# Kernel optimization log

Hardware: AMD Instinct MI355X
Metric: run time of the kernel (lower is better)

Reference implementation:

```python
import jax, jax.numpy as jnp
import numpy as np

# norse LIFParameters defaults with method='super', alpha=100
TAU_SYN_INV = 200.0
TAU_MEM_INV = 100.0
V_LEAK = 0.0
V_TH = 1.0
V_RESET = 0.0
ALPHA = 100.0
DT = 0.001
SEQ_LENGTH = 100

@jax.custom_vjp
def super_spike(x):
    return (x > 0).astype(x.dtype)

def _ss_fwd(x):
    return super_spike(x), x

def _ss_bwd(x, g):
    # SuperSpike surrogate: dz/dx = 1 / (alpha*|x| + 1)^2
    return (g / (ALPHA * jnp.abs(x) + 1.0) ** 2,)

super_spike.defvjp(_ss_fwd, _ss_bwd)

def lif_step(inp, v, i):
    v_dec = v + DT * TAU_MEM_INV * ((V_LEAK - v) + i)
    i_dec = i * (1.0 - DT * TAU_SYN_INV)
    z = super_spike(v_dec - V_TH)
    v_new = (1.0 - z) * v_dec + z * V_RESET
    i_new = i_dec + inp
    return z, v_new, i_new

def setup_inputs() -> dict:
    key = jax.random.key(0)
    ks = jax.random.split(key, 5)
    B, F, H, C = 16384, 256, 256, 10
    x = jax.random.normal(ks[0], (B, F), dtype=jnp.float32)
    W_hidden = jax.random.normal(ks[1], (H, F), dtype=jnp.float32) / np.sqrt(F)
    b_hidden = jax.random.normal(ks[2], (H,), dtype=jnp.float32) * 0.01
    W_readout = jax.random.normal(ks[3], (C, H), dtype=jnp.float32) / np.sqrt(H)
    b_readout = jax.random.normal(ks[4], (C,), dtype=jnp.float32) * 0.01
    return {"x": x, "W_hidden": W_hidden, "b_hidden": b_hidden,
            "W_readout": W_readout, "b_readout": b_readout}

def reference(x, W_hidden, b_hidden, W_readout, b_readout):
    B, F = x.shape
    H = W_hidden.shape[0]
    z0 = jnp.zeros((B, F), x.dtype)
    z1 = jnp.zeros((B, H), x.dtype)

    def step(carry, _):
        v1, i1, v2, i2, acc = carry
        # input LIF cell (same input current x at every timestep)
        z, v1, i1 = lif_step(x, v1, i1)
        h = jnp.einsum('bf,hf->bh', z, W_hidden) + b_hidden
        # output LIF cell
        z2, v2, i2 = lif_step(h, v2, i2)
        return (v1, i1, v2, i2, acc + z2), None

    carry0 = (z0, z0, z1, z1, z1)
    (v1, i1, v2, i2, acc), _ = jax.lax.scan(step, carry0, None, length=SEQ_LENGTH)
    mean_spikes = acc / SEQ_LENGTH  # == outputs.mean(0)
    return jnp.einsum('bh,ch->bc', mean_spikes, W_readout) + b_readout
```

## Files before the change

### kernel.cpp

```cpp
#include <hip/hip_runtime.h>
#include <hip/hip_fp16.h>
#include <stdint.h>


#define BB 16384
#define FF 256
#define HH 256
#define CC 10
#define TT 100

typedef __attribute__((ext_vector_type(4))) int int4v;

__global__ __launch_bounds__(256) void spike_gen(
    const float* __restrict__ x, unsigned long long* __restrict__ Z) {
  const int lane = threadIdx.x & 63;
  const int wv   = threadIdx.x >> 6;
  const int b0   = blockIdx.x * 8 + wv * 2;
  const float K_VM = (float)(0.001 * 100.0);
  const float K_ID = (float)(1.0 - 0.001 * 200.0);

  float v[8], cur[8], xv[8];
#pragma unroll
  for (int jb = 0; jb < 2; ++jb)
#pragma unroll
    for (int js = 0; js < 4; ++js) {
      const int idx = jb * 4 + js;
      xv[idx] = x[(size_t)(b0 + jb) * FF + js * 64 + lane];
      v[idx] = 0.0f; cur[idx] = 0.0f;
    }

  const bool s0 = (lane & 1) != 0, s1 = (lane & 2) != 0, s2 = (lane & 4) != 0;
  unsigned long long* zp = Z + (size_t)b0 * 4;

  for (int t = 0; t < TT; ++t) {
    unsigned long long bal[8];
#pragma unroll
    for (int idx = 0; idx < 8; ++idx) {
      float vd   = __fadd_rn(v[idx], __fmul_rn(K_VM, __fadd_rn(-v[idx], cur[idx])));
      float idec = __fmul_rn(cur[idx], K_ID);
      bool z = (vd > 1.0f);
      bal[idx] = __ballot(z);
      v[idx]   = z ? 0.0f : vd;
      cur[idx] = __fadd_rn(idec, xv[idx]);
    }
    unsigned long long m0 = s0 ? bal[1] : bal[0];
    unsigned long long m1 = s0 ? bal[3] : bal[2];
    unsigned long long m2 = s0 ? bal[5] : bal[4];
    unsigned long long m3 = s0 ? bal[7] : bal[6];
    unsigned long long n0 = s1 ? m1 : m0;
    unsigned long long n1 = s1 ? m3 : m2;
    unsigned long long m  = s2 ? n1 : n0;
    if (lane < 8) zp[(size_t)t * (BB * 4) + lane] = m;
  }
}

__global__ __launch_bounds__(256, 4) void snn_main(
    const uint32_t* __restrict__ Z, const float* __restrict__ Wh,
    const float* __restrict__ bh, const float* __restrict__ Wr,
    const float* __restrict__ br, float* __restrict__ out) {
  __shared__ __align__(16) char WS[32768];

  const int tid = threadIdx.x;
  const int bx  = blockIdx.x;
  const int hc  = bx & 3;
  const int bc  = bx >> 2;
  const int h0  = hc * 64;
  const int b0  = bc * 64;

  {
    int4v* ws4 = (int4v*)WS;
#pragma unroll
    for (int half = 0; half < 4; ++half) {
      const int u  = tid + half * 256;
      const int rr = u >> 4;
      const int q  = u & 15;
      const int s  = q >> 2, kq = q & 3;
      const int nt = rr >> 4, n = rr & 15;
      const float* wp = Wh + (size_t)(h0 + rr) * FF + s * 64 + kq * 16;
      uint32_t pa[4], pb[4];
#pragma unroll
      for (int c4 = 0; c4 < 4; ++c4) {
        float4 w4 = *(const float4*)(wp + c4 * 4);
        float wf[4] = {w4.x, w4.y, w4.z, w4.w};
        uint32_t ua = 0, ub = 0;
#pragma unroll
        for (int e = 0; e < 4; ++e) {
          float af = rintf(wf[e] * 256.0f);
          af = fminf(fmaxf(af, -127.0f), 127.0f);
          float bf = rintf(__builtin_fmaf(af, -64.0f, wf[e] * 16384.0f));
          bf = fminf(fmaxf(bf, -127.0f), 127.0f);
          ua |= ((uint32_t)((int)af) & 255u) << (8 * e);
          ub |= ((uint32_t)((int)bf) & 255u) << (8 * e);
        }
        pa[c4] = ua; pb[c4] = ub;
      }
      ws4[((nt * 2 + 0) * 4 + s) * 64 + kq * 16 + n] = *(int4v*)pa;
      ws4[((nt * 2 + 1) * 4 + s) * 64 + kq * 16 + n] = *(int4v*)pb;
    }
  }
  __syncthreads();

  const int lane = tid & 63;
  const int bsub = tid >> 6;
  const int col  = lane & 15;
  const int quad = lane >> 4;
  const bool qhi = (quad & 2) != 0;
  const uint32_t shl16 = (quad & 1) * 16;

  const int brow = b0 + bsub * 16 + col;

  const float K_VM = (float)(0.001 * 100.0);
  const float K_ID = (float)(1.0 - 0.001 * 200.0);

  float v2[4][4], ii[4][4];
  uint32_t sc[4];
#pragma unroll
  for (int nt = 0; nt < 4; ++nt) {
    sc[nt] = 0u;
#pragma unroll
    for (int r = 0; r < 4; ++r) { v2[nt][r] = 0.f; ii[nt][r] = 0.f; }
  }

  float bias[4];
#pragma unroll
  for (int nt = 0; nt < 4; ++nt) bias[nt] = bh[h0 + nt * 16 + col];

  uint32_t hwS0[2], hwS1[2], hwS2[2], hwS3[2];
  const uint32_t* zrow = Z + (size_t)brow * 8;

  auto load_hw = [&](int tgi) {
#pragma unroll
    for (int j = 0; j < 2; ++j) {
      const uint32_t* p = zrow + ((size_t)tgi * 2 + j) * (size_t)(BB * 8);
      uint4 a = *(const uint4*)p;
      uint4 b4 = *(const uint4*)(p + 4);
      hwS0[j] = (qhi ? a.y : a.x) >> shl16;
      hwS1[j] = (qhi ? a.w : a.z) >> shl16;
      hwS2[j] = (qhi ? b4.y : b4.x) >> shl16;
      hwS3[j] = (qhi ? b4.w : b4.z) >> shl16;
    }
  };
  load_hw(0);

  const char* wsl = WS + lane * 16;

#pragma unroll 1
  for (int tg = 0; tg < TT / 2; ++tg) {
    int4v acc[2][4];
#pragma unroll
    for (int j = 0; j < 2; ++j)
#pragma unroll
      for (int nt = 0; nt < 4; ++nt)
        acc[j][nt] = (int4v){0, 0, 0, 0};

#pragma unroll 1
    for (int s = 0; s < 4; ++s) {
      const int4v* bp = (const int4v*)(wsl + s * 1024);
      int4v Ba[4], Bb[4];
#pragma unroll
      for (int nt = 0; nt < 4; ++nt) {
        Ba[nt] = bp[(nt * 2 + 0) * 256];
        Bb[nt] = bp[(nt * 2 + 1) * 256];
      }
#pragma unroll
      for (int j = 0; j < 2; ++j) {
        uint32_t t0 = (s & 1) ? hwS1[j] : hwS0[j];
        uint32_t t1 = (s & 1) ? hwS3[j] : hwS2[j];
        uint32_t h16 = (s & 2) ? t1 : t0;
        int4v za, zb_;
#pragma unroll
        for (int p = 0; p < 4; ++p) {
          uint32_t nib = (h16 >> (4 * p)) & 15u;
          uint32_t zbyte = __umul24(nib, 0x204081u) & 0x01010101u;
          zb_[p] = (int)zbyte;
          za[p]  = (int)(zbyte << 6);
        }
#pragma unroll
        for (int nt = 0; nt < 4; ++nt) {
          acc[j][nt] = __builtin_amdgcn_mfma_i32_16x16x64_i8(
              za, Ba[nt], acc[j][nt], 0, 0, 0);
          acc[j][nt] = __builtin_amdgcn_mfma_i32_16x16x64_i8(
              zb_, Bb[nt], acc[j][nt], 0, 0, 0);
        }
      }
    }

    if (tg < TT / 2 - 1) load_hw(tg + 1);

#pragma unroll
    for (int j = 0; j < 2; ++j) {
#pragma unroll
      for (int nt = 0; nt < 4; ++nt) {
#pragma unroll
        for (int r = 0; r < 4; ++r) {
          float h  = __builtin_fmaf((float)acc[j][nt][r], 6.103515625e-05f,
                                    bias[nt]);
          float vv = v2[nt][r], ci = ii[nt][r];
          float vd   = __fadd_rn(vv, __fmul_rn(K_VM, __fadd_rn(-vv, ci)));
          float idec = __fmul_rn(ci, K_ID);
          bool z = (vd > 1.0f);
          v2[nt][r] = z ? 0.0f : vd;
          ii[nt][r] = __fadd_rn(idec, h);
          sc[nt] += (z ? 1u : 0u) << (8 * r);
        }
      }
    }
  }

  float mean[4][4];
#pragma unroll
  for (int nt = 0; nt < 4; ++nt)
#pragma unroll
    for (int r = 0; r < 4; ++r)
      mean[nt][r] = __fdiv_rn((float)((sc[nt] >> (8 * r)) & 255u), 100.0f);

#pragma unroll 1
  for (int c = 0; c < CC; ++c) {
    float wc[4];
#pragma unroll
    for (int nt = 0; nt < 4; ++nt) wc[nt] = Wr[c * HH + h0 + nt * 16 + col];
#pragma unroll
    for (int r = 0; r < 4; ++r) {
      float s = 0.f;
#pragma unroll
      for (int nt = 0; nt < 4; ++nt) s = fmaf(mean[nt][r], wc[nt], s);
      s += __shfl_xor(s, 1);
      s += __shfl_xor(s, 2);
      s += __shfl_xor(s, 4);
      s += __shfl_xor(s, 8);
      if (col == 0) {
        int b = b0 + bsub * 16 + quad * 4 + r;
        float add = s + ((hc == 0) ? br[c] : 0.0f);
        atomicAdd(&out[b * CC + c], add);
      }
    }
  }
}

extern "C" void kernel_launch(void* const* d_in, const int* in_sizes, int n_in,
                              void* d_out, int out_size, void* d_ws, size_t ws_size,
                              hipStream_t stream) {
  const float* x  = (const float*)d_in[0];
  const float* Wh = (const float*)d_in[1];
  const float* bh = (const float*)d_in[2];
  const float* Wr = (const float*)d_in[3];
  const float* br = (const float*)d_in[4];
  float* out = (float*)d_out;

  unsigned long long* Z = (unsigned long long*)d_ws;

  hipMemsetAsync(d_out, 0, (size_t)out_size * sizeof(float), stream);
  spike_gen<<<BB / 8, 256, 0, stream>>>(x, Z);
  snn_main<<<1024, 256, 0, stream>>>((const uint32_t*)Z, Wh, bh, Wr, br, out);
}
```

Baseline: 389.8 us.

## Software-pipeline MFMA matmul with LIF update and batch spike stores

The main kernel splits the two-timestep accumulator into separate A and B accumulators. The MFMA k-loop for the next timestep is issued before the LIF update of the previous one, so VALU work can overlap with matrix ops. B-operand LDS loads are split into two halves to lower register pressure. The spike generator now buffers four timesteps of ballot masks before storing them, which groups the global writes but holds more live registers.

```diff
diff --git a/kernel.cpp b/kernel.cpp
--- a/kernel.cpp
+++ b/kernel.cpp
@@ -32,25 +32,33 @@
   const bool s0 = (lane & 1) != 0, s1 = (lane & 2) != 0, s2 = (lane & 4) != 0;
   unsigned long long* zp = Z + (size_t)b0 * 4;
 
-  for (int t = 0; t < TT; ++t) {
-    unsigned long long bal[8];
-#pragma unroll
-    for (int idx = 0; idx < 8; ++idx) {
-      float vd   = __fadd_rn(v[idx], __fmul_rn(K_VM, __fadd_rn(-v[idx], cur[idx])));
-      float idec = __fmul_rn(cur[idx], K_ID);
-      bool z = (vd > 1.0f);
-      bal[idx] = __ballot(z);
-      v[idx]   = z ? 0.0f : vd;
-      cur[idx] = __fadd_rn(idec, xv[idx]);
-    }
-    unsigned long long m0 = s0 ? bal[1] : bal[0];
-    unsigned long long m1 = s0 ? bal[3] : bal[2];
-    unsigned long long m2 = s0 ? bal[5] : bal[4];
-    unsigned long long m3 = s0 ? bal[7] : bal[6];
-    unsigned long long n0 = s1 ? m1 : m0;
-    unsigned long long n1 = s1 ? m3 : m2;
-    unsigned long long m  = s2 ? n1 : n0;
-    if (lane < 8) zp[(size_t)t * (BB * 4) + lane] = m;
+  for (int t4 = 0; t4 < TT; t4 += 4) {
+    unsigned long long mq[4];
+#pragma unroll
+    for (int k = 0; k < 4; ++k) {
+      unsigned long long bal[8];
+#pragma unroll
+      for (int idx = 0; idx < 8; ++idx) {
+        float vd   = __fadd_rn(v[idx], __fmul_rn(K_VM, __fadd_rn(-v[idx], cur[idx])));
+        float idec = __fmul_rn(cur[idx], K_ID);
+        bool z = (vd > 1.0f);
+        bal[idx] = __ballot(z);
+        v[idx]   = z ? 0.0f : vd;
+        cur[idx] = __fadd_rn(idec, xv[idx]);
+      }
+      unsigned long long m0 = s0 ? bal[1] : bal[0];
+      unsigned long long m1 = s0 ? bal[3] : bal[2];
+      unsigned long long m2 = s0 ? bal[5] : bal[4];
+      unsigned long long m3 = s0 ? bal[7] : bal[6];
+      unsigned long long n0 = s1 ? m1 : m0;
+      unsigned long long n1 = s1 ? m3 : m2;
+      mq[k] = s2 ? n1 : n0;
+    }
+    if (lane < 8) {
+#pragma unroll
+      for (int k = 0; k < 4; ++k)
+        zp[(size_t)(t4 + k) * (BB * 4) + lane] = mq[k];
+    }
   }
 }
 
@@ -125,7 +133,7 @@
 #pragma unroll
   for (int nt = 0; nt < 4; ++nt) bias[nt] = bh[h0 + nt * 16 + col];
 
-  uint32_t hwS0[2], hwS1[2], hwS2[2], hwS3[2];
+  uint32_t hw0[2], hw1[2], hw2[2], hw3[2];
   const uint32_t* zrow = Z + (size_t)brow * 8;
 
   auto load_hw = [&](int tgi) {
@@ -134,77 +142,87 @@
       const uint32_t* p = zrow + ((size_t)tgi * 2 + j) * (size_t)(BB * 8);
       uint4 a = *(const uint4*)p;
       uint4 b4 = *(const uint4*)(p + 4);
-      hwS0[j] = (qhi ? a.y : a.x) >> shl16;
-      hwS1[j] = (qhi ? a.w : a.z) >> shl16;
-      hwS2[j] = (qhi ? b4.y : b4.x) >> shl16;
-      hwS3[j] = (qhi ? b4.w : b4.z) >> shl16;
+      hw0[j] = (qhi ? a.y : a.x) >> shl16;
+      hw1[j] = (qhi ? a.w : a.z) >> shl16;
+      hw2[j] = (qhi ? b4.y : b4.x) >> shl16;
+      hw3[j] = (qhi ? b4.w : b4.z) >> shl16;
     }
   };
   load_hw(0);
 
   const char* wsl = WS + lane * 16;
 
-#pragma unroll 1
-  for (int tg = 0; tg < TT / 2; ++tg) {
-    int4v acc[2][4];
-#pragma unroll
-    for (int j = 0; j < 2; ++j)
-#pragma unroll
-      for (int nt = 0; nt < 4; ++nt)
-        acc[j][nt] = (int4v){0, 0, 0, 0};
-
+  int4v accA[4], accB[4];
+
+  auto zero4 = [](int4v (&ac)[4]) {
+#pragma unroll
+    for (int nt = 0; nt < 4; ++nt) ac[nt] = (int4v){0, 0, 0, 0};
+  };
+
+  auto kloop = [&](int4v (&ac)[4], uint32_t a0, uint32_t a1, uint32_t a2,
+                   uint32_t a3) {
 #pragma unroll 1
     for (int s = 0; s < 4; ++s) {
       const int4v* bp = (const int4v*)(wsl + s * 1024);
-      int4v Ba[4], Bb[4];
-#pragma unroll
-      for (int nt = 0; nt < 4; ++nt) {
-        Ba[nt] = bp[(nt * 2 + 0) * 256];
-        Bb[nt] = bp[(nt * 2 + 1) * 256];
-      }
-#pragma unroll
-      for (int j = 0; j < 2; ++j) {
-        uint32_t t0 = (s & 1) ? hwS1[j] : hwS0[j];
-        uint32_t t1 = (s & 1) ? hwS3[j] : hwS2[j];
-        uint32_t h16 = (s & 2) ? t1 : t0;
-        int4v za, zb_;
-#pragma unroll
-        for (int p = 0; p < 4; ++p) {
-          uint32_t nib = (h16 >> (4 * p)) & 15u;
-          uint32_t zbyte = __umul24(nib, 0x204081u) & 0x01010101u;
-          zb_[p] = (int)zbyte;
-          za[p]  = (int)(zbyte << 6);
-        }
-#pragma unroll
-        for (int nt = 0; nt < 4; ++nt) {
-          acc[j][nt] = __builtin_amdgcn_mfma_i32_16x16x64_i8(
-              za, Ba[nt], acc[j][nt], 0, 0, 0);
-          acc[j][nt] = __builtin_amdgcn_mfma_i32_16x16x64_i8(
-              zb_, Bb[nt], acc[j][nt], 0, 0, 0);
-        }
-      }
-    }
-
+      uint32_t t0 = (s & 1) ? a1 : a0;
+      uint32_t t1 = (s & 1) ? a3 : a2;
+      uint32_t h16 = (s & 2) ? t1 : t0;
+      int4v za, zb_;
+#pragma unroll
+      for (int p = 0; p < 4; ++p) {
+        uint32_t nib = (h16 >> (4 * p)) & 15u;
+        uint32_t zbyte = __umul24(nib, 0x204081u) & 0x01010101u;
+        zb_[p] = (int)zbyte;
+        za[p]  = (int)(zbyte << 6);
+      }
+      int4v Ba[4];
+#pragma unroll
+      for (int nt = 0; nt < 4; ++nt) Ba[nt] = bp[(nt * 2 + 0) * 256];
+#pragma unroll
+      for (int nt = 0; nt < 4; ++nt)
+        ac[nt] = __builtin_amdgcn_mfma_i32_16x16x64_i8(za, Ba[nt], ac[nt],
+                                                       0, 0, 0);
+      int4v Bb[4];
+#pragma unroll
+      for (int nt = 0; nt < 4; ++nt) Bb[nt] = bp[(nt * 2 + 1) * 256];
+#pragma unroll
+      for (int nt = 0; nt < 4; ++nt)
+        ac[nt] = __builtin_amdgcn_mfma_i32_16x16x64_i8(zb_, Bb[nt], ac[nt],
+                                                       0, 0, 0);
+    }
+  };
+
+  auto lif = [&](int4v (&ac)[4]) {
+#pragma unroll
+    for (int nt = 0; nt < 4; ++nt) {
+#pragma unroll
+      for (int r = 0; r < 4; ++r) {
+        float h  = __builtin_fmaf((float)ac[nt][r], 6.103515625e-05f,
+                                  bias[nt]);
+        float vv = v2[nt][r], ci = ii[nt][r];
+        float vd   = __fadd_rn(vv, __fmul_rn(K_VM, __fadd_rn(-vv, ci)));
+        float idec = __fmul_rn(ci, K_ID);
+        bool z = (vd > 1.0f);
+        v2[nt][r] = z ? 0.0f : vd;
+        ii[nt][r] = __fadd_rn(idec, h);
+        sc[nt] += (z ? 1u : 0u) << (8 * r);
+      }
+    }
+  };
+
+  zero4(accA);
+  kloop(accA, hw0[0], hw1[0], hw2[0], hw3[0]);
+#pragma unroll 1
+  for (int tg = 0; tg < TT / 2; ++tg) {
+    zero4(accB);
+    kloop(accB, hw0[1], hw1[1], hw2[1], hw3[1]);
     if (tg < TT / 2 - 1) load_hw(tg + 1);
-
-#pragma unroll
-    for (int j = 0; j < 2; ++j) {
-#pragma unroll
-      for (int nt = 0; nt < 4; ++nt) {
-#pragma unroll
-        for (int r = 0; r < 4; ++r) {
-          float h  = __builtin_fmaf((float)acc[j][nt][r], 6.103515625e-05f,
-                                    bias[nt]);
-          float vv = v2[nt][r], ci = ii[nt][r];
-          float vd   = __fadd_rn(vv, __fmul_rn(K_VM, __fadd_rn(-vv, ci)));
-          float idec = __fmul_rn(ci, K_ID);
-          bool z = (vd > 1.0f);
-          v2[nt][r] = z ? 0.0f : vd;
-          ii[nt][r] = __fadd_rn(idec, h);
-          sc[nt] += (z ? 1u : 0u) << (8 * r);
-        }
-      }
-    }
+    lif(accA);
+    if (tg < TT / 2 - 1) {
+      zero4(accA);
+      kloop(accA, hw0[0], hw1[0], hw2[0], hw3[0]);
+    }
+    lif(accB);
   }
 
   float mean[4][4];
```

After: 443.7 us. 1.14x slower.

## Repack spike bitmasks so each lane loads only its own 8 bytes, double-buffer loads

Applied to the files above, without the earlier changes.

The spike generator now transposes ballot words so each quad's 16-bit slices for all four feature segments sit in one contiguous 64-bit word, and it batches stores across four timesteps. The main kernel then loads a single uint2 per lane per timestep instead of two uint4 loads with select and shift logic. The main loop is unrolled by two with ping-pong register buffers so the next timestep's spike load is issued before the current MFMA work. This reduces global load traffic and address/select ALU work, at the cost of extra bit shuffling in the cheap generator kernel.

```diff
diff --git a/kernel.cpp b/kernel.cpp
--- a/kernel.cpp
+++ b/kernel.cpp
@@ -32,25 +32,46 @@
   const bool s0 = (lane & 1) != 0, s1 = (lane & 2) != 0, s2 = (lane & 4) != 0;
   unsigned long long* zp = Z + (size_t)b0 * 4;
 
-  for (int t = 0; t < TT; ++t) {
-    unsigned long long bal[8];
-#pragma unroll
-    for (int idx = 0; idx < 8; ++idx) {
-      float vd   = __fadd_rn(v[idx], __fmul_rn(K_VM, __fadd_rn(-v[idx], cur[idx])));
-      float idec = __fmul_rn(cur[idx], K_ID);
-      bool z = (vd > 1.0f);
-      bal[idx] = __ballot(z);
-      v[idx]   = z ? 0.0f : vd;
-      cur[idx] = __fadd_rn(idec, xv[idx]);
-    }
-    unsigned long long m0 = s0 ? bal[1] : bal[0];
-    unsigned long long m1 = s0 ? bal[3] : bal[2];
-    unsigned long long m2 = s0 ? bal[5] : bal[4];
-    unsigned long long m3 = s0 ? bal[7] : bal[6];
-    unsigned long long n0 = s1 ? m1 : m0;
-    unsigned long long n1 = s1 ? m3 : m2;
-    unsigned long long m  = s2 ? n1 : n0;
-    if (lane < 8) zp[(size_t)t * (BB * 4) + lane] = m;
+  for (int t4 = 0; t4 < TT; t4 += 4) {
+    unsigned long long mq[4];
+#pragma unroll
+    for (int k = 0; k < 4; ++k) {
+      unsigned long long bal[8];
+#pragma unroll
+      for (int idx = 0; idx < 8; ++idx) {
+        float vd   = __fadd_rn(v[idx], __fmul_rn(K_VM, __fadd_rn(-v[idx], cur[idx])));
+        float idec = __fmul_rn(cur[idx], K_ID);
+        bool z = (vd > 1.0f);
+        bal[idx] = __ballot(z);
+        v[idx]   = z ? 0.0f : vd;
+        cur[idx] = __fadd_rn(idec, xv[idx]);
+      }
+      unsigned long long W[8];
+#pragma unroll
+      for (int jb = 0; jb < 2; ++jb) {
+        unsigned long long a0 = bal[jb * 4 + 0], a1 = bal[jb * 4 + 1];
+        unsigned long long a2 = bal[jb * 4 + 2], a3 = bal[jb * 4 + 3];
+#pragma unroll
+        for (int q = 0; q < 4; ++q) {
+          W[jb * 4 + q] = ((a0 >> (16 * q)) & 0xffffull)
+                        | (((a1 >> (16 * q)) & 0xffffull) << 16)
+                        | (((a2 >> (16 * q)) & 0xffffull) << 32)
+                        | (((a3 >> (16 * q)) & 0xffffull) << 48);
+        }
+      }
+      unsigned long long m0 = s0 ? W[1] : W[0];
+      unsigned long long m1 = s0 ? W[3] : W[2];
+      unsigned long long m2 = s0 ? W[5] : W[4];
+      unsigned long long m3 = s0 ? W[7] : W[6];
+      unsigned long long n0 = s1 ? m1 : m0;
+      unsigned long long n1 = s1 ? m3 : m2;
+      mq[k] = s2 ? n1 : n0;
+    }
+    if (lane < 8) {
+#pragma unroll
+      for (int k = 0; k < 4; ++k)
+        zp[(size_t)(t4 + k) * (BB * 4) + lane] = mq[k];
+    }
   }
 }
 
@@ -104,8 +125,6 @@
   const int bsub = tid >> 6;
   const int col  = lane & 15;
   const int quad = lane >> 4;
-  const bool qhi = (quad & 2) != 0;
-  const uint32_t shl16 = (quad & 1) * 16;
 
   const int brow = b0 + bsub * 16 + col;
 
@@ -125,28 +144,21 @@
 #pragma unroll
   for (int nt = 0; nt < 4; ++nt) bias[nt] = bh[h0 + nt * 16 + col];
 
-  uint32_t hwS0[2], hwS1[2], hwS2[2], hwS3[2];
-  const uint32_t* zrow = Z + (size_t)brow * 8;
-
-  auto load_hw = [&](int tgi) {
-#pragma unroll
-    for (int j = 0; j < 2; ++j) {
-      const uint32_t* p = zrow + ((size_t)tgi * 2 + j) * (size_t)(BB * 8);
-      uint4 a = *(const uint4*)p;
-      uint4 b4 = *(const uint4*)(p + 4);
-      hwS0[j] = (qhi ? a.y : a.x) >> shl16;
-      hwS1[j] = (qhi ? a.w : a.z) >> shl16;
-      hwS2[j] = (qhi ? b4.y : b4.x) >> shl16;
-      hwS3[j] = (qhi ? b4.w : b4.z) >> shl16;
-    }
+  const char* zq = (const char*)Z + (size_t)brow * 32 + quad * 8;
+  uint2 zrA[2], zrB[2];
+
+  auto load_z = [&](int tgi, uint2 (&zr)[2]) {
+#pragma unroll
+    for (int j = 0; j < 2; ++j)
+      zr[j] = *(const uint2*)(zq + ((size_t)tgi * 2 + j) * (size_t)(BB * 32));
   };
-  load_hw(0);
+  load_z(0, zrA);
 
   const char* wsl = WS + lane * 16;
 
-#pragma unroll 1
-  for (int tg = 0; tg < TT / 2; ++tg) {
-    int4v acc[2][4];
+  int4v acc[2][4];
+
+  auto body = [&](const uint2 (&zr)[2]) {
 #pragma unroll
     for (int j = 0; j < 2; ++j)
 #pragma unroll
@@ -162,11 +174,11 @@
         Ba[nt] = bp[(nt * 2 + 0) * 256];
         Bb[nt] = bp[(nt * 2 + 1) * 256];
       }
+      const uint32_t sh = (uint32_t)(s & 1) * 16;
 #pragma unroll
       for (int j = 0; j < 2; ++j) {
-        uint32_t t0 = (s & 1) ? hwS1[j] : hwS0[j];
-        uint32_t t1 = (s & 1) ? hwS3[j] : hwS2[j];
-        uint32_t h16 = (s & 2) ? t1 : t0;
+        uint32_t w   = (s & 2) ? zr[j].y : zr[j].x;
+        uint32_t h16 = w >> sh;
         int4v za, zb_;
 #pragma unroll
         for (int p = 0; p < 4; ++p) {
@@ -184,8 +196,6 @@
         }
       }
     }
-
-    if (tg < TT / 2 - 1) load_hw(tg + 1);
 
 #pragma unroll
     for (int j = 0; j < 2; ++j) {
@@ -205,6 +215,14 @@
         }
       }
     }
+  };
+
+#pragma unroll 1
+  for (int it = 0; it < TT / 4; ++it) {
+    load_z(2 * it + 1, zrB);
+    body(zrA);
+    if (it < TT / 4 - 1) load_z(2 * it + 2, zrA);
+    body(zrB);
   }
 
   float mean[4][4];
```

After: 443.8 us. 13.9% more time.

## Stagger timestep pairing across blocks and batch spike-plane stores

Applied to the files above, without the earlier changes.

In the main kernel, about half the blocks now pair timesteps at an odd offset: they run a redundant matmul for t=0 and a padded pass at t=99. This staggers the MFMA-heavy phase against the scalar LIF phase across neighbouring blocks, meant to improve overlap of matrix and vector work on each CU. The spike generator buffers four timesteps of ballot masks and writes them together to reduce store interleaving. The stagger adds two extra MFMA passes for those blocks and more control complexity.

```diff
diff --git a/kernel.cpp b/kernel.cpp
--- a/kernel.cpp
+++ b/kernel.cpp
@@ -32,25 +32,33 @@
   const bool s0 = (lane & 1) != 0, s1 = (lane & 2) != 0, s2 = (lane & 4) != 0;
   unsigned long long* zp = Z + (size_t)b0 * 4;
 
-  for (int t = 0; t < TT; ++t) {
-    unsigned long long bal[8];
-#pragma unroll
-    for (int idx = 0; idx < 8; ++idx) {
-      float vd   = __fadd_rn(v[idx], __fmul_rn(K_VM, __fadd_rn(-v[idx], cur[idx])));
-      float idec = __fmul_rn(cur[idx], K_ID);
-      bool z = (vd > 1.0f);
-      bal[idx] = __ballot(z);
-      v[idx]   = z ? 0.0f : vd;
-      cur[idx] = __fadd_rn(idec, xv[idx]);
-    }
-    unsigned long long m0 = s0 ? bal[1] : bal[0];
-    unsigned long long m1 = s0 ? bal[3] : bal[2];
-    unsigned long long m2 = s0 ? bal[5] : bal[4];
-    unsigned long long m3 = s0 ? bal[7] : bal[6];
-    unsigned long long n0 = s1 ? m1 : m0;
-    unsigned long long n1 = s1 ? m3 : m2;
-    unsigned long long m  = s2 ? n1 : n0;
-    if (lane < 8) zp[(size_t)t * (BB * 4) + lane] = m;
+  for (int t4 = 0; t4 < TT; t4 += 4) {
+    unsigned long long mq[4];
+#pragma unroll
+    for (int k = 0; k < 4; ++k) {
+      unsigned long long bal[8];
+#pragma unroll
+      for (int idx = 0; idx < 8; ++idx) {
+        float vd   = __fadd_rn(v[idx], __fmul_rn(K_VM, __fadd_rn(-v[idx], cur[idx])));
+        float idec = __fmul_rn(cur[idx], K_ID);
+        bool z = (vd > 1.0f);
+        bal[idx] = __ballot(z);
+        v[idx]   = z ? 0.0f : vd;
+        cur[idx] = __fadd_rn(idec, xv[idx]);
+      }
+      unsigned long long m0 = s0 ? bal[1] : bal[0];
+      unsigned long long m1 = s0 ? bal[3] : bal[2];
+      unsigned long long m2 = s0 ? bal[5] : bal[4];
+      unsigned long long m3 = s0 ? bal[7] : bal[6];
+      unsigned long long n0 = s1 ? m1 : m0;
+      unsigned long long n1 = s1 ? m3 : m2;
+      mq[k] = s2 ? n1 : n0;
+    }
+    if (lane < 8) {
+#pragma unroll
+      for (int k = 0; k < 4; ++k)
+        zp[(size_t)(t4 + k) * (BB * 4) + lane] = mq[k];
+    }
   }
 }
 
@@ -125,34 +133,28 @@
 #pragma unroll
   for (int nt = 0; nt < 4; ++nt) bias[nt] = bh[h0 + nt * 16 + col];
 
-  uint32_t hwS0[2], hwS1[2], hwS2[2], hwS3[2];
+  uint32_t hw0[2], hw1[2], hw2[2], hw3[2];
   const uint32_t* zrow = Z + (size_t)brow * 8;
 
-  auto load_hw = [&](int tgi) {
-#pragma unroll
-    for (int j = 0; j < 2; ++j) {
-      const uint32_t* p = zrow + ((size_t)tgi * 2 + j) * (size_t)(BB * 8);
-      uint4 a = *(const uint4*)p;
-      uint4 b4 = *(const uint4*)(p + 4);
-      hwS0[j] = (qhi ? a.y : a.x) >> shl16;
-      hwS1[j] = (qhi ? a.w : a.z) >> shl16;
-      hwS2[j] = (qhi ? b4.y : b4.x) >> shl16;
-      hwS3[j] = (qhi ? b4.w : b4.z) >> shl16;
-    }
+  auto load_plane = [&](int t, int j) {
+    const uint32_t* p = zrow + (size_t)t * (size_t)(BB * 8);
+    uint4 a = *(const uint4*)p;
+    uint4 b4 = *(const uint4*)(p + 4);
+    hw0[j] = (qhi ? a.y : a.x) >> shl16;
+    hw1[j] = (qhi ? a.w : a.z) >> shl16;
+    hw2[j] = (qhi ? b4.y : b4.x) >> shl16;
+    hw3[j] = (qhi ? b4.w : b4.z) >> shl16;
   };
-  load_hw(0);
 
   const char* wsl = WS + lane * 16;
-
-#pragma unroll 1
-  for (int tg = 0; tg < TT / 2; ++tg) {
-    int4v acc[2][4];
+  int4v acc[2][4];
+
+  auto kloop2 = [&]() {
 #pragma unroll
     for (int j = 0; j < 2; ++j)
 #pragma unroll
       for (int nt = 0; nt < 4; ++nt)
         acc[j][nt] = (int4v){0, 0, 0, 0};
-
 #pragma unroll 1
     for (int s = 0; s < 4; ++s) {
       const int4v* bp = (const int4v*)(wsl + s * 1024);
@@ -164,8 +166,8 @@
       }
 #pragma unroll
       for (int j = 0; j < 2; ++j) {
-        uint32_t t0 = (s & 1) ? hwS1[j] : hwS0[j];
-        uint32_t t1 = (s & 1) ? hwS3[j] : hwS2[j];
+        uint32_t t0 = (s & 1) ? hw1[j] : hw0[j];
+        uint32_t t1 = (s & 1) ? hw3[j] : hw2[j];
         uint32_t h16 = (s & 2) ? t1 : t0;
         int4v za, zb_;
 #pragma unroll
@@ -184,26 +186,49 @@
         }
       }
     }
-
-    if (tg < TT / 2 - 1) load_hw(tg + 1);
-
-#pragma unroll
-    for (int j = 0; j < 2; ++j) {
-#pragma unroll
-      for (int nt = 0; nt < 4; ++nt) {
-#pragma unroll
-        for (int r = 0; r < 4; ++r) {
-          float h  = __builtin_fmaf((float)acc[j][nt][r], 6.103515625e-05f,
-                                    bias[nt]);
-          float vv = v2[nt][r], ci = ii[nt][r];
-          float vd   = __fadd_rn(vv, __fmul_rn(K_VM, __fadd_rn(-vv, ci)));
-          float idec = __fmul_rn(ci, K_ID);
-          bool z = (vd > 1.0f);
-          v2[nt][r] = z ? 0.0f : vd;
-          ii[nt][r] = __fadd_rn(idec, h);
-          sc[nt] += (z ? 1u : 0u) << (8 * r);
-        }
-      }
+  };
+
+  auto lifp = [&](int j) {
+#pragma unroll
+    for (int nt = 0; nt < 4; ++nt) {
+#pragma unroll
+      for (int r = 0; r < 4; ++r) {
+        float h  = __builtin_fmaf((float)acc[j][nt][r], 6.103515625e-05f,
+                                  bias[nt]);
+        float vv = v2[nt][r], ci = ii[nt][r];
+        float vd   = __fadd_rn(vv, __fmul_rn(K_VM, __fadd_rn(-vv, ci)));
+        float idec = __fmul_rn(ci, K_ID);
+        bool z = (vd > 1.0f);
+        v2[nt][r] = z ? 0.0f : vd;
+        ii[nt][r] = __fadd_rn(idec, h);
+        sc[nt] += (z ? 1u : 0u) << (8 * r);
+      }
+    }
+  };
+
+  const int stag = ((bx >> 5) ^ (bx >> 8)) & 1;
+
+  if (stag) {
+    load_plane(0, 0); load_plane(0, 1);
+    kloop2();
+    load_plane(1, 0); load_plane(2, 1);
+    lifp(0);
+#pragma unroll 1
+    for (int k = 0; k < 49; ++k) {
+      kloop2();
+      if (k < 48) { load_plane(3 + 2 * k, 0); load_plane(4 + 2 * k, 1); }
+      else        { load_plane(99, 0);         load_plane(99, 1); }
+      lifp(0); lifp(1);
+    }
+    kloop2();
+    lifp(0);
+  } else {
+    load_plane(0, 0); load_plane(1, 1);
+#pragma unroll 1
+    for (int k = 0; k < 50; ++k) {
+      kloop2();
+      if (k < 49) { load_plane(2 + 2 * k, 0); load_plane(3 + 2 * k, 1); }
+      lifp(0); lifp(1);
     }
   }
 
```

Measured after the change: 396.1 us. Within noise of the previous version (+1.6%).
